# Performance work log

Hardware: AMD Instinct MI355X
Metric: run time of the kernel (lower is better)

The kernel has to match this reference:

```python
import jax, jax.numpy as jnp
import numpy as np

N, K, F = 8192, 64, 128  # nodes, neighbors (nb_sparse), feature map width


def setup_inputs() -> dict:
    key = jax.random.key(0)
    k1, k2, k3, k4 = jax.random.split(key, 4)
    return {
        "emb_in": jax.random.normal(k1, (N, F), dtype=jnp.float32),
        "sum_weights": jax.random.uniform(k2, (N,), dtype=jnp.float32),
        "idx_in": jax.random.randint(k3, (N, K - 1), 0, N),  # neighbor indices (KNN output)
        "edge_out": jax.random.normal(k4, (N, K), dtype=jnp.float32),  # edge-net output, resized to [N, K]
    }


def reference(emb_in, sum_weights, idx_in, edge_out):
    n, f = emb_in.shape
    k = idx_in.shape[1] + 1
    # append self-index as the last neighbor (as in make_samples)
    idx = jnp.concatenate([idx_in, jnp.arange(n, dtype=idx_in.dtype)[:, None]], axis=1)  # [N, K]

    # --- make_samples: gather-concat, fully vectorized over nodes ---
    node = jnp.broadcast_to(emb_in[:, None, :], (n, k, f))          # node repeated k times
    neighbors = emb_in[idx]                                          # [N, K, F] gather
    edge_wts = sum_weights[idx][..., None]                           # [N, K, 1]
    samples = jnp.concatenate([node, neighbors, edge_wts], axis=-1).reshape(n * k, 2 * f + 1)

    # --- get_adj: sequential row build; `line` carries over between rows (faithful to torch code) ---
    def step(line, xs):
        idx_i, e_i = xs
        line = line.at[idx_i].set(e_i)
        return line, line

    line0 = jnp.zeros((n,), dtype=edge_out.dtype)
    _, adj = jax.lax.scan(step, line0, (idx, edge_out))  # adj: [N, N]

    return samples, adj
```

## Files before the change

kernel.cpp:

```cpp
#include <hip/hip_runtime.h>
#include <cstdint>

#define N_NODES 8192
#define K_NB    64
#define F_DIM   128
#define SAMP_W  (2 * F_DIM + 1)
#define ROWS_PER_BLK 64
#define NBLK (N_NODES / ROWS_PER_BLK)
#define CW   2048
#define NCHUNK (N_NODES / CW)

static __device__ __forceinline__ unsigned long long pack_uv(unsigned int ord, float v) {
    return ((unsigned long long)ord << 32) | (unsigned long long)__float_as_uint(v);
}
static __device__ __forceinline__ float unpack_v(unsigned long long p) {
    return __uint_as_float((unsigned int)(p & 0xffffffffULL));
}

__global__ __launch_bounds__(256) void samples_kernel(
    const float* __restrict__ emb, const float* __restrict__ sw,
    const int* __restrict__ idx, float* __restrict__ out)
{
    const int i = blockIdx.x;
    const int t = threadIdx.x;
    float nd = 0.0f;
    if (t < F_DIM) nd = emb[i * F_DIM + t];
    const int rowbase = i * (K_NB * SAMP_W);
    for (int j = 0; j < K_NB; ++j) {
        const int c = (j < K_NB - 1) ? idx[i * (K_NB - 1) + j] : i;
        const int base = rowbase + j * SAMP_W;
        if (t < F_DIM) {
            out[base + t] = nd;
            if (t == 0) out[base + 2 * F_DIM] = sw[c];
        } else {
            out[base + t] = emb[c * F_DIM + (t - F_DIM)];
        }
    }
}

__global__ __launch_bounds__(256) void p1_kernel(
    const int* __restrict__ idx, const float* __restrict__ edge,
    unsigned long long* __restrict__ S)
{
    __shared__ unsigned long long line[N_NODES];
    const int b = blockIdx.x;
    const int t = threadIdx.x;
    for (int k = t; k < N_NODES; k += 256) line[k] = 0ULL;
    __syncthreads();
    for (int u = t; u < ROWS_PER_BLK * K_NB; u += 256) {
        const int r = b * ROWS_PER_BLK + (u >> 6);
        const int j = u & 63;
        const int c = (j < K_NB - 1) ? idx[r * (K_NB - 1) + j] : r;
        const float v = edge[r * K_NB + j];
        atomicMax(&line[c], pack_uv((unsigned)(r * K_NB + j + 1), v));
    }
    __syncthreads();
    for (int k = t; k < N_NODES; k += 256) S[b * N_NODES + k] = line[k];
}

__global__ __launch_bounds__(256) void p2_kernel(
    const unsigned long long* __restrict__ S, float* __restrict__ carry)
{
    const int c = blockIdx.x * 256 + threadIdx.x;
    unsigned long long run = 0ULL;
    for (int b = 0; b < NBLK; ++b) {
        carry[b * N_NODES + c] = unpack_v(run);
        const unsigned long long s = S[b * N_NODES + c];
        if (s != 0ULL) run = s;
    }
}

__global__ __launch_bounds__(256) void p3_kernel(
    const int* __restrict__ idx, const float* __restrict__ edge,
    const float* __restrict__ carry, float* __restrict__ adj)
{
    __shared__ unsigned long long line[CW];
    const int b  = blockIdx.x;
    const int c0 = blockIdx.y * CW;
    const int t  = threadIdx.x;
    for (int k = t; k < CW; k += 256)
        line[k] = pack_uv(0u, carry[b * N_NODES + c0 + k]);
    __syncthreads();
    for (int rr = 0; rr < ROWS_PER_BLK; ++rr) {
        const int r = b * ROWS_PER_BLK + rr;
        if (t < K_NB) {
            const int j = t;
            const int c = (j < K_NB - 1) ? idx[r * (K_NB - 1) + j] : r;
            const unsigned int cc = (unsigned)(c - c0);
            if (cc < (unsigned)CW) {
                const float v = edge[r * K_NB + j];
                atomicMax(&line[cc], pack_uv((unsigned)(r * K_NB + j + 1), v));
            }
        }
        __syncthreads();
        const int rowbase = r * N_NODES + c0;
        for (int k = t; k < CW; k += 256)
            adj[rowbase + k] = unpack_v(line[k]);
        __syncthreads();
    }
}

extern "C" void kernel_launch(void* const* d_in, const int* in_sizes, int n_in,
                              void* d_out, int out_size, void* d_ws, size_t ws_size,
                              hipStream_t stream)
{
    const float* emb  = (const float*)d_in[0];
    const float* sw   = (const float*)d_in[1];
    const int*   idx  = (const int*)d_in[2];
    const float* edge = (const float*)d_in[3];

    float* out      = (float*)d_out;
    float* samples  = out;
    float* adj      = out + (size_t)N_NODES * K_NB * SAMP_W;

    unsigned long long* S = (unsigned long long*)d_out;
    float* carry = (float*)((char*)d_out + (size_t)NBLK * N_NODES * 8);

    p1_kernel<<<NBLK, 256, 0, stream>>>(idx, edge, S);
    p2_kernel<<<N_NODES / 256, 256, 0, stream>>>(S, carry);
    p3_kernel<<<dim3(NBLK, NCHUNK), 256, 0, stream>>>(idx, edge, carry, adj);
    samples_kernel<<<N_NODES, 256, 0, stream>>>(emb, sw, idx, samples);
}
```

Before: 1.007 ms.

## Split samples kernel over neighbor chunks, prefetch indices, use nontemporal stores

The samples kernel now launches a 2D grid where each block handles 8 neighbors, preloading their indices and gathered values before issuing nontemporal stores. The adjacency build halves rows per block and column chunk width, and prefetches the next row's index and edge value while the current row is stored. Adjacency writes become unrolled nontemporal stores, and the carry scan loop is unrolled. The aim is more parallelism and memory-level overlap with less cache pollution from the large streaming outputs. The cost is twice as many carry/S blocks for the scan, which overlaps the samples region in workspace.

```diff
diff --git a/kernel.cpp b/kernel.cpp
--- a/kernel.cpp
+++ b/kernel.cpp
@@ -5,10 +5,12 @@
 #define K_NB    64
 #define F_DIM   128
 #define SAMP_W  (2 * F_DIM + 1)
-#define ROWS_PER_BLK 64
-#define NBLK (N_NODES / ROWS_PER_BLK)
-#define CW   2048
-#define NCHUNK (N_NODES / CW)
+#define RPB     32
+#define NBLK    (N_NODES / RPB)
+#define CW      1024
+#define NCHUNK  (N_NODES / CW)
+
+typedef float v4f __attribute__((ext_vector_type(4)));
 
 static __device__ __forceinline__ unsigned long long pack_uv(unsigned int ord, float v) {
     return ((unsigned long long)ord << 32) | (unsigned long long)__float_as_uint(v);
@@ -21,20 +23,35 @@
     const float* __restrict__ emb, const float* __restrict__ sw,
     const int* __restrict__ idx, float* __restrict__ out)
 {
-    const int i = blockIdx.x;
-    const int t = threadIdx.x;
-    float nd = 0.0f;
-    if (t < F_DIM) nd = emb[i * F_DIM + t];
-    const int rowbase = i * (K_NB * SAMP_W);
-    for (int j = 0; j < K_NB; ++j) {
-        const int c = (j < K_NB - 1) ? idx[i * (K_NB - 1) + j] : i;
-        const int base = rowbase + j * SAMP_W;
-        if (t < F_DIM) {
-            out[base + t] = nd;
-            if (t == 0) out[base + 2 * F_DIM] = sw[c];
-        } else {
-            out[base + t] = emb[c * F_DIM + (t - F_DIM)];
+    const int i  = blockIdx.x;
+    const int j0 = blockIdx.y * 8;
+    const int t  = threadIdx.x;
+
+    int c[8];
+#pragma unroll
+    for (int jj = 0; jj < 8; ++jj) {
+        const int j = j0 + jj;
+        c[jj] = (j < K_NB - 1) ? idx[i * (K_NB - 1) + j] : i;
+    }
+    const int rowbase = i * (K_NB * SAMP_W) + j0 * SAMP_W;
+
+    if (t < F_DIM) {
+        const float nd = emb[i * F_DIM + t];
+#pragma unroll
+        for (int jj = 0; jj < 8; ++jj) {
+            const int base = rowbase + jj * SAMP_W;
+            __builtin_nontemporal_store(nd, &out[base + t]);
+            if (t == 0)
+                __builtin_nontemporal_store(sw[c[jj]], &out[base + 2 * F_DIM]);
         }
+    } else {
+        float v[8];
+#pragma unroll
+        for (int jj = 0; jj < 8; ++jj)
+            v[jj] = emb[c[jj] * F_DIM + (t - F_DIM)];
+#pragma unroll
+        for (int jj = 0; jj < 8; ++jj)
+            __builtin_nontemporal_store(v[jj], &out[rowbase + jj * SAMP_W + t]);
     }
 }
 
@@ -47,12 +64,12 @@
     const int t = threadIdx.x;
     for (int k = t; k < N_NODES; k += 256) line[k] = 0ULL;
     __syncthreads();
-    for (int u = t; u < ROWS_PER_BLK * K_NB; u += 256) {
-        const int r = b * ROWS_PER_BLK + (u >> 6);
+    for (int u = t; u < RPB * K_NB; u += 256) {
+        const int r = b * RPB + (u >> 6);
         const int j = u & 63;
-        const int c = (j < K_NB - 1) ? idx[r * (K_NB - 1) + j] : r;
+        const int cc = (j < K_NB - 1) ? idx[r * (K_NB - 1) + j] : r;
         const float v = edge[r * K_NB + j];
-        atomicMax(&line[c], pack_uv((unsigned)(r * K_NB + j + 1), v));
+        atomicMax(&line[cc], pack_uv((unsigned)(r * K_NB + j + 1), v));
     }
     __syncthreads();
     for (int k = t; k < N_NODES; k += 256) S[b * N_NODES + k] = line[k];
@@ -63,6 +80,7 @@
 {
     const int c = blockIdx.x * 256 + threadIdx.x;
     unsigned long long run = 0ULL;
+#pragma unroll 8
     for (int b = 0; b < NBLK; ++b) {
         carry[b * N_NODES + c] = unpack_v(run);
         const unsigned long long s = S[b * N_NODES + c];
@@ -78,25 +96,47 @@
     const int b  = blockIdx.x;
     const int c0 = blockIdx.y * CW;
     const int t  = threadIdx.x;
+
     for (int k = t; k < CW; k += 256)
         line[k] = pack_uv(0u, carry[b * N_NODES + c0 + k]);
+
+    int   cN = 0;
+    float vN = 0.0f;
+    {
+        const int r0 = b * RPB;
+        if (t < K_NB) {
+            cN = (t < K_NB - 1) ? idx[r0 * (K_NB - 1) + t] : r0;
+            vN = edge[r0 * K_NB + t];
+        }
+    }
     __syncthreads();
-    for (int rr = 0; rr < ROWS_PER_BLK; ++rr) {
-        const int r = b * ROWS_PER_BLK + rr;
+
+    for (int rr = 0; rr < RPB; ++rr) {
+        const int r = b * RPB + rr;
         if (t < K_NB) {
-            const int j = t;
-            const int c = (j < K_NB - 1) ? idx[r * (K_NB - 1) + j] : r;
-            const unsigned int cc = (unsigned)(c - c0);
-            if (cc < (unsigned)CW) {
-                const float v = edge[r * K_NB + j];
-                atomicMax(&line[cc], pack_uv((unsigned)(r * K_NB + j + 1), v));
-            }
+            const unsigned cc = (unsigned)(cN - c0);
+            if (cc < (unsigned)CW)
+                atomicMax(&line[cc], pack_uv((unsigned)(r * K_NB + t + 1), vN));
         }
         __syncthreads();
+
+        const float x0 = unpack_v(line[t]);
+        const float x1 = unpack_v(line[t + 256]);
+        const float x2 = unpack_v(line[t + 512]);
+        const float x3 = unpack_v(line[t + 768]);
+
+        if (rr + 1 < RPB && t < K_NB) {
+            const int r2 = r + 1;
+            cN = (t < K_NB - 1) ? idx[r2 * (K_NB - 1) + t] : r2;
+            vN = edge[r2 * K_NB + t];
+        }
+        __syncthreads();
+
         const int rowbase = r * N_NODES + c0;
-        for (int k = t; k < CW; k += 256)
-            adj[rowbase + k] = unpack_v(line[k]);
-        __syncthreads();
+        __builtin_nontemporal_store(x0, &adj[rowbase + t]);
+        __builtin_nontemporal_store(x1, &adj[rowbase + t + 256]);
+        __builtin_nontemporal_store(x2, &adj[rowbase + t + 512]);
+        __builtin_nontemporal_store(x3, &adj[rowbase + t + 768]);
     }
 }
 
@@ -109,9 +149,9 @@
     const int*   idx  = (const int*)d_in[2];
     const float* edge = (const float*)d_in[3];
 
-    float* out      = (float*)d_out;
-    float* samples  = out;
-    float* adj      = out + (size_t)N_NODES * K_NB * SAMP_W;
+    float* out     = (float*)d_out;
+    float* samples = out;
+    float* adj     = out + (size_t)N_NODES * K_NB * SAMP_W;
 
     unsigned long long* S = (unsigned long long*)d_out;
     float* carry = (float*)((char*)d_out + (size_t)NBLK * N_NODES * 8);
@@ -119,5 +159,5 @@
     p1_kernel<<<NBLK, 256, 0, stream>>>(idx, edge, S);
     p2_kernel<<<N_NODES / 256, 256, 0, stream>>>(S, carry);
     p3_kernel<<<dim3(NBLK, NCHUNK), 256, 0, stream>>>(idx, edge, carry, adj);
-    samples_kernel<<<N_NODES, 256, 0, stream>>>(emb, sw, idx, samples);
+    samples_kernel<<<dim3(N_NODES, 8), 256, 0, stream>>>(emb, sw, idx, samples);
 }
```

Result: slower. 1.029 ms (+2.2%).
